# Optimization experiments

Measured on AMD Instinct MI355X. Metric: run time of the kernel, lower is better.

Reference implementation:

```python
import jax, jax.numpy as jnp
import numpy as np

B, T, D = 2, 2048, 1024
H = 4
KD = int(D * 0.5)      # total key dim = 512
VD = int(D * 1.0)      # total value dim = 1024
DK, DV = KD // H, VD // H  # per-head: 128, 256
CHUNK = 64
LOW_RANK = 16          # gate_low_rank_dim
NORMALIZER = 16.0      # gate_logit_normalizer
EPS = 1e-6


def setup_inputs() -> dict:
    key = jax.random.key(0)
    ks = jax.random.split(key, 10)
    def w(k, shape):
        return jax.random.normal(k, shape, jnp.float32) / np.sqrt(shape[0]).astype(np.float32)
    return {
        "x": jax.random.normal(ks[0], (B, T, D), jnp.float32),
        "Wq": w(ks[1], (D, KD)),
        "Wk": w(ks[2], (D, KD)),
        "Wv": w(ks[3], (D, VD)),
        "Wg": w(ks[4], (D, VD)),          # output gate projection
        "Wgk1": w(ks[5], (D, LOW_RANK)),  # low-rank gate proj (no bias)
        "Wgk2": w(ks[6], (LOW_RANK, KD)),
        "bgk2": jax.random.normal(ks[7], (KD,), jnp.float32) * 0.1,
        "gnorm_w": jnp.ones((DV,), jnp.float32),  # FusedRMSNormSwishGate weight
        "Wo": w(ks[8], (VD, D)),
    }


def reference(x, Wq, Wk, Wv, Wg, Wgk1, Wgk2, bgk2, gnorm_w, Wo):
    scale = DK ** -0.5
    NC = T // CHUNK
    # [B,T,d] -> [NC,B,H,C,d_head]
    to_heads = lambda a, d: a.reshape(B, NC, CHUNK, H, d).transpose(1, 0, 3, 2, 4)
    q = to_heads(x @ Wq, DK)
    k = to_heads(x @ Wk, DK)
    v = to_heads(x @ Wv, DV)
    # per-key log decay gate: logsigmoid(low-rank proj) / normalizer
    gk = jax.nn.log_sigmoid((x @ Wgk1) @ Wgk2 + bgk2) / NORMALIZER
    G = jnp.cumsum(to_heads(gk, DK), axis=3)  # inclusive cumsum within chunk

    def chunk_step(S, inp):
        k_c, v_c, G_c = inp                       # [B,H,C,DK],[B,H,C,DV],[B,H,C,DK]
        G_last = G_c[:, :, -1, :]                 # [B,H,DK] total chunk decay
        k_bar = k_c * jnp.exp(G_last[:, :, None, :] - G_c)  # decay pos->chunk end
        S_new = jnp.exp(G_last)[..., None] * S + jnp.einsum('bhck,bhcv->bhkv', k_bar, v_c)
        return S_new, S                           # emit state at chunk START

    S0 = jnp.zeros((B, H, DK, DV), x.dtype)
    _, S_prev = jax.lax.scan(chunk_step, S0, (k, v, G))  # [NC,B,H,DK,DV]

    qg = q * jnp.exp(G) * scale                   # decay-scaled queries
    o_inter = jnp.einsum('nbhck,nbhkv->nbhcv', qg, S_prev)
    kg = k * jnp.exp(-G)
    A = jnp.einsum('nbhik,nbhjk->nbhij', qg, kg)  # intra-chunk scores
    A = jnp.where(jnp.tril(jnp.ones((CHUNK, CHUNK), bool)), A, 0.0)
    o = o_inter + jnp.einsum('nbhij,nbhjv->nbhiv', A, v)  # [NC,B,H,C,DV]
    o = o.transpose(1, 0, 3, 2, 4).reshape(B, T, H, DV)

    # fused gated RMSNorm: rmsnorm(o)*weight * swish(g), then output proj
    g = (x @ Wg).reshape(B, T, H, DV)
    o = o * jax.lax.rsqrt(jnp.mean(o * o, axis=-1, keepdims=True) + EPS) * gnorm_w
    o = o * (g * jax.nn.sigmoid(g))
    return o.reshape(B, T, VD) @ Wo
```

## Files before the change

### kernel.cpp

```cpp
#include <hip/hip_runtime.h>
#include <hip/hip_bf16.h>

#define BDIM 2
#define TDIM 2048
#define DDIM 1024
#define HH 4
#define KD 512
#define VD 1024
#define DK 128
#define DV 256
#define NC 32
#define CHUNKC 64
#define MTOT (BDIM*TDIM)
#define NALL 3584
#define STRIDE_ST ((size_t)BDIM*HH*DK*DV)

typedef __bf16 bf16x8 __attribute__((ext_vector_type(8)));
typedef float  f32x4  __attribute__((ext_vector_type(4)));
typedef __hip_bfloat16 hbf;

__device__ __forceinline__ void async_copy16(const void* g, void* l) {
  __builtin_amdgcn_global_load_lds(
      (const __attribute__((address_space(1))) void*)g,
      (__attribute__((address_space(3))) void*)l, 16, 0, 0);
}

__global__ void cast_bf16_kernel(const float* __restrict__ src, hbf* __restrict__ dst) {
  int t = blockIdx.x*256 + threadIdx.x;
  float4 v = ((const float4*)src)[t];
  union { hbf h[4]; uint2 u; } o;
  o.h[0] = __float2bfloat16(v.x); o.h[1] = __float2bfloat16(v.y);
  o.h[2] = __float2bfloat16(v.z); o.h[3] = __float2bfloat16(v.w);
  ((uint2*)dst)[t] = o.u;
}

__global__ void prep_weights(const float* __restrict__ Wq, const float* __restrict__ Wk,
                             const float* __restrict__ Wv, const float* __restrict__ Wg,
                             const float* __restrict__ Wo, const float* __restrict__ W1,
                             const float* __restrict__ W2,
                             hbf* __restrict__ wtall, hbf* __restrict__ wto) {
  __shared__ float tile[32][33];
  const int n0 = blockIdx.x*32, k0 = blockIdx.y*32;
  const int tx = threadIdx.x & 31, ty = threadIdx.x >> 5;
  if (n0 >= 1024 && n0 < 1536) {
    #pragma unroll
    for (int r = ty; r < 32; r += 8) {
      int n = n0 - 1024 + r, k = k0 + tx;
      float s = 0.f;
      #pragma unroll
      for (int j = 0; j < 16; ++j) s += W1[(size_t)k*16 + j] * W2[(size_t)j*KD + n];
      wtall[(size_t)(n0 + r)*DDIM + k] = __float2bfloat16(s);
    }
    return;
  }
  const float* W; int Nsrc, nloc; hbf* outp; int orow;
  if      (n0 < 512)  { W = Wq; Nsrc = 512;  nloc = n0;        outp = wtall; orow = n0; }
  else if (n0 < 1024) { W = Wk; Nsrc = 512;  nloc = n0 - 512;  outp = wtall; orow = n0; }
  else if (n0 < 2560) { W = Wv; Nsrc = 1024; nloc = n0 - 1536; outp = wtall; orow = n0; }
  else if (n0 < 3584) { W = Wg; Nsrc = 1024; nloc = n0 - 2560; outp = wtall; orow = n0; }
  else                { W = Wo; Nsrc = 1024; nloc = n0 - 3584; outp = wto;   orow = n0 - 3584; }
  #pragma unroll
  for (int r = ty; r < 32; r += 8)
    tile[r][tx] = W[(size_t)(k0 + r)*Nsrc + nloc + tx];
  __syncthreads();
  #pragma unroll
  for (int r = ty; r < 32; r += 8)
    outp[(size_t)(orow + r)*DDIM + k0 + tx] = __float2bfloat16(tile[tx][r]);
}

template <int MODE>
__global__ __launch_bounds__(256) void gemm_bt(const hbf* __restrict__ A,
                                               const hbf* __restrict__ Bt,
                                               float* __restrict__ Cf,
                                               hbf* __restrict__ Cq,
                                               hbf* __restrict__ Cv,
                                               int M, int N, int K) {
  __shared__ hbf As0[128][32], As1[128][32];
  __shared__ hbf Bs0[128][32], Bs1[128][32];
  const int t = threadIdx.x;
  const int w = t >> 6, l = t & 63;
  const int lr = l >> 2;
  const int srcc = (((l & 3) - (l >> 4)) & 3) * 8;
  const int lane16 = l & 15, quad = l >> 4;
  const int sw = (lane16 >> 2) & 3;
  const int row0 = blockIdx.y*128, col0 = blockIdx.x*128;
  const int mb = (w >> 1)*64, nb = (w & 1)*64;

  const hbf* ga = A  + (size_t)(row0 + w*32 + lr)*K + srcc;
  const hbf* gb = Bt + (size_t)(col0 + w*32 + lr)*K + srcc;
  hbf* la0 = &As0[w*32][0];   hbf* la1 = &As0[w*32 + 16][0];
  hbf* la2 = &As1[w*32][0];   hbf* la3 = &As1[w*32 + 16][0];
  hbf* lb0 = &Bs0[w*32][0];   hbf* lb1 = &Bs0[w*32 + 16][0];
  hbf* lb2 = &Bs1[w*32][0];   hbf* lb3 = &Bs1[w*32 + 16][0];
  const size_t rstep = (size_t)16*K;

  f32x4 acc[4][4] = {};
  for (int k0 = 0; k0 < K; k0 += 64) {
    async_copy16(ga,              la0);
    async_copy16(ga + rstep,      la1);
    async_copy16(ga + 32,         la2);
    async_copy16(ga + rstep + 32, la3);
    async_copy16(gb,              lb0);
    async_copy16(gb + rstep,      lb1);
    async_copy16(gb + 32,         lb2);
    async_copy16(gb + rstep + 32, lb3);
    ga += 64; gb += 64;
    __syncthreads();
    {
      bf16x8 af[4], bfr[4];
      #pragma unroll
      for (int i = 0; i < 4; ++i)
        af[i] = *(const bf16x8*)&As0[mb + i*16 + lane16][((quad + sw) & 3)*8];
      #pragma unroll
      for (int j = 0; j < 4; ++j)
        bfr[j] = *(const bf16x8*)&Bs0[nb + j*16 + lane16][((quad + sw) & 3)*8];
      #pragma unroll
      for (int i = 0; i < 4; ++i)
        #pragma unroll
        for (int j = 0; j < 4; ++j)
          acc[i][j] = __builtin_amdgcn_mfma_f32_16x16x32_bf16(af[i], bfr[j], acc[i][j], 0, 0, 0);
    }
    {
      bf16x8 af[4], bfr[4];
      #pragma unroll
      for (int i = 0; i < 4; ++i)
        af[i] = *(const bf16x8*)&As1[mb + i*16 + lane16][((quad + sw) & 3)*8];
      #pragma unroll
      for (int j = 0; j < 4; ++j)
        bfr[j] = *(const bf16x8*)&Bs1[nb + j*16 + lane16][((quad + sw) & 3)*8];
      #pragma unroll
      for (int i = 0; i < 4; ++i)
        #pragma unroll
        for (int j = 0; j < 4; ++j)
          acc[i][j] = __builtin_amdgcn_mfma_f32_16x16x32_bf16(af[i], bfr[j], acc[i][j], 0, 0, 0);
    }
    __syncthreads();
  }
  #pragma unroll
  for (int i = 0; i < 4; ++i)
    #pragma unroll
    for (int j = 0; j < 4; ++j)
      #pragma unroll
      for (int r = 0; r < 4; ++r) {
        int m = row0 + mb + i*16 + quad*4 + r;
        int n = col0 + nb + j*16 + lane16;
        float v = acc[i][j][r];
        if (MODE == 0) {
          Cf[(size_t)m*N + n] = v;
        } else {
          if (n < 1024)       Cq[(size_t)m*1024 + n] = __float2bfloat16(v);
          else if (n < 1536)  Cf[(size_t)m*512  + n - 1024] = v;
          else                Cv[(size_t)m*2048 + n - 1536] = __float2bfloat16(v);
        }
      }
}

__global__ __launch_bounds__(256) void gate_kernel(const float* __restrict__ Gpre,
                                                   const hbf* __restrict__ qkbf,
                                                   const float* __restrict__ bias,
                                                   hbf* __restrict__ qgb,
                                                   hbf* __restrict__ kgb,
                                                   hbf* __restrict__ kbarb,
                                                   float* __restrict__ dec) {
  __shared__ float buf[CHUNKC][128];
  const int h  = blockIdx.x & 3;
  const int nc = (blockIdx.x >> 2) & 31;
  const int b  = blockIdx.x >> 7;
  const int t = threadIdx.x;
  const int bc = b*TDIM + nc*CHUNKC;
  const int col0 = h*128;
  #pragma unroll
  for (int i = 0; i < 32; ++i) {
    int idx = t + 256*i;
    int c = idx >> 7, col = idx & 127;
    float s = Gpre[(size_t)(bc + c)*KD + col0 + col] + bias[col0 + col];
    buf[c][col] = (fminf(s, 0.f) - log1pf(expf(-fabsf(s)))) * (1.0f/16.0f);
  }
  __syncthreads();
  if (t < 128) {
    float acc = 0.f;
    #pragma unroll
    for (int c = 0; c < CHUNKC; ++c) { acc += buf[c][t]; buf[c][t] = acc; }
    dec[((size_t)nc*8 + b*HH + h)*DK + t] = expf(acc);
  }
  __syncthreads();
  const float scale = 0.088388347648318447f;
  #pragma unroll
  for (int i = 0; i < 16; ++i) {
    int idx = t + 256*i;
    int c = idx >> 6, cp = (idx & 63)*2;
    float g0 = buf[c][cp], g1 = buf[c][cp + 1];
    float gl0 = buf[63][cp], gl1 = buf[63][cp + 1];
    const size_t qoff = (size_t)(bc + c)*1024 + col0 + cp;
    uint qu = *(const uint*)(qkbf + qoff);
    uint ku = *(const uint*)(qkbf + qoff + 512);
    float q0 = __bfloat162float(((const hbf*)&qu)[0]);
    float q1 = __bfloat162float(((const hbf*)&qu)[1]);
    float k0 = __bfloat162float(((const hbf*)&ku)[0]);
    float k1 = __bfloat162float(((const hbf*)&ku)[1]);
    union { hbf h2[2]; uint u; } o1, o2, o3;
    o1.h2[0] = __float2bfloat16(q0 * expf(g0) * scale);
    o1.h2[1] = __float2bfloat16(q1 * expf(g1) * scale);
    o2.h2[0] = __float2bfloat16(k0 * expf(-g0));
    o2.h2[1] = __float2bfloat16(k1 * expf(-g1));
    o3.h2[0] = __float2bfloat16(k0 * expf(gl0 - g0));
    o3.h2[1] = __float2bfloat16(k1 * expf(gl1 - g1));
    const size_t ooff = (size_t)(bc + c)*KD + col0 + cp;
    *(uint*)(qgb + ooff)   = o1.u;
    *(uint*)(kgb + ooff)   = o2.u;
    *(uint*)(kbarb + ooff) = o3.u;
  }
}

__global__ __launch_bounds__(256) void state_chunk_kernel(const hbf* __restrict__ kbarb,
                                                          const hbf* __restrict__ vgbf,
                                                          hbf* __restrict__ Ub) {
  const int bh = blockIdx.x & 7;
  const int nc = blockIdx.x >> 3;
  const int b = bh >> 2, h = bh & 3;
  const int t = threadIdx.x;
  const int w = t >> 6, l = t & 63;
  const int lane16 = l & 15, quad = l >> 4;
  __shared__ hbf kbarT[DK][72];
  __shared__ hbf vT[DV][72];
  const int bc = b*TDIM + nc*CHUNKC;
  #pragma unroll
  for (int i = 0; i < 32; ++i) {
    int idx = t + 256*i;
    int c = idx >> 7, kk = idx & 127;
    kbarT[kk][c] = kbarb[(size_t)(bc + c)*KD + h*DK + kk];
  }
  #pragma unroll
  for (int i = 0; i < 64; ++i) {
    int idx = t + 256*i;
    int c = idx >> 8, col = idx & 255;
    vT[col][c] = vgbf[(size_t)(bc + c)*2048 + h*DV + col];
  }
  __syncthreads();
  f32x4 acc[4][8] = {};
  #pragma unroll
  for (int kc = 0; kc < 2; ++kc) {
    bf16x8 av[4], bk[8];
    #pragma unroll
    for (int i = 0; i < 4; ++i)
      av[i] = *(const bf16x8*)&vT[w*64 + i*16 + lane16][kc*32 + quad*8];
    #pragma unroll
    for (int j = 0; j < 8; ++j)
      bk[j] = *(const bf16x8*)&kbarT[j*16 + lane16][kc*32 + quad*8];
    #pragma unroll
    for (int i = 0; i < 4; ++i)
      #pragma unroll
      for (int j = 0; j < 8; ++j)
        acc[i][j] = __builtin_amdgcn_mfma_f32_16x16x32_bf16(av[i], bk[j], acc[i][j], 0, 0, 0);
  }
  hbf* ub = Ub + ((size_t)nc*8 + bh)*((size_t)DK*DV);
  #pragma unroll
  for (int i = 0; i < 4; ++i)
    #pragma unroll
    for (int j = 0; j < 8; ++j)
      #pragma unroll
      for (int r = 0; r < 4; ++r) {
        int v = w*64 + i*16 + quad*4 + r;
        int k = j*16 + lane16;
        ub[(size_t)v*DK + k] = __float2bfloat16(acc[i][j][r]);
      }
}

__global__ __launch_bounds__(256) void state_scan_kernel(const hbf* __restrict__ Ub,
                                                         const float* __restrict__ dec,
                                                         hbf* __restrict__ Spb) {
  const int p = blockIdx.x*256 + threadIdx.x;
  const size_t e = (size_t)p*2;
  const int k = (int)(e & 127);
  const int bh = (int)(e >> 15);
  float S0 = 0.f, S1 = 0.f;
  for (int nc = 0; nc < NC; ++nc) {
    const size_t off = (size_t)nc*STRIDE_ST + e;
    uint uu = *(const uint*)(Ub + off);
    hbf u0 = *(const hbf*)&uu;
    hbf u1 = *((const hbf*)&uu + 1);
    union { hbf h[2]; uint u; } ov;
    ov.h[0] = __float2bfloat16(S0); ov.h[1] = __float2bfloat16(S1);
    *(uint*)(Spb + off) = ov.u;
    float2 d = *(const float2*)(dec + ((size_t)nc*8 + bh)*DK + k);
    S0 = S0 * d.x + __bfloat162float(u0);
    S1 = S1 * d.y + __bfloat162float(u1);
  }
}

__global__ __launch_bounds__(256) void out_kernel(const hbf* __restrict__ qgb,
                                                  const hbf* __restrict__ kgb,
                                                  const hbf* __restrict__ vgbf,
                                                  const hbf* __restrict__ Spb,
                                                  const float* __restrict__ gnw,
                                                  hbf* __restrict__ obf) {
  const int blk = blockIdx.x;
  const int h = blk & 3, b = (blk >> 2) & 1, nc = blk >> 3;
  const int t = threadIdx.x;
  const int w = t >> 6, l = t & 63;
  const int lane16 = l & 15, quad = l >> 4;

  __shared__ __align__(16) unsigned char smem[64768];
  hbf (*qgs)[136] = (hbf(*)[136])(smem);
  hbf (*Ald)[72]  = (hbf(*)[72]) (smem + 17408);
  hbf (*kgs)[136] = (hbf(*)[136])(smem + 26624);
  hbf (*vT)[72]   = (hbf(*)[72]) (smem + 26624);
  float* ssum     = (float*)     (smem + 63488);
  float* invb     = (float*)     (smem + 64512);

  const int bc = b*TDIM + nc*CHUNKC;

  #pragma unroll
  for (int i = 0; i < 4; ++i) {
    int idx = t + 256*i;
    int c = idx >> 4, ch = (idx & 15)*8;
    *(uint4*)&qgs[c][ch] = *(const uint4*)(qgb + (size_t)(bc + c)*KD + h*DK + ch);
    *(uint4*)&kgs[c][ch] = *(const uint4*)(kgb + (size_t)(bc + c)*KD + h*DK + ch);
  }
  __syncthreads();

  f32x4 acc1[4] = {};
  #pragma unroll
  for (int kc = 0; kc < 4; ++kc) {
    bf16x8 af = *(const bf16x8*)&qgs[w*16 + lane16][kc*32 + quad*8];
    #pragma unroll
    for (int j = 0; j < 4; ++j) {
      bf16x8 bf = *(const bf16x8*)&kgs[j*16 + lane16][kc*32 + quad*8];
      acc1[j] = __builtin_amdgcn_mfma_f32_16x16x32_bf16(af, bf, acc1[j], 0, 0, 0);
    }
  }
  __syncthreads();

  #pragma unroll
  for (int j = 0; j < 4; ++j)
    #pragma unroll
    for (int r = 0; r < 4; ++r) {
      int cr = w*16 + quad*4 + r;
      int cc = j*16 + lane16;
      Ald[cr][cc] = __float2bfloat16(cc <= cr ? acc1[j][r] : 0.f);
    }
  #pragma unroll
  for (int i = 0; i < 64; ++i) {
    int e = t + 256*i;
    int c = e >> 8, col = e & 255;
    vT[col][c] = vgbf[(size_t)(bc + c)*2048 + h*DV + col];
  }
  __syncthreads();

  const hbf* SpB = Spb + ((size_t)nc*8 + (b*HH + h))*((size_t)DK*DV);
  f32x4 acc[4][4] = {};
  #pragma unroll
  for (int kc = 0; kc < 4; ++kc) {
    bf16x8 af[4], bs[4];
    #pragma unroll
    for (int i = 0; i < 4; ++i)
      af[i] = *(const bf16x8*)&qgs[i*16 + lane16][kc*32 + quad*8];
    #pragma unroll
    for (int j = 0; j < 4; ++j) {
      int n = w*64 + j*16 + lane16;
      bs[j] = *(const bf16x8*)(SpB + (size_t)n*DK + kc*32 + quad*8);
    }
    #pragma unroll
    for (int i = 0; i < 4; ++i)
      #pragma unroll
      for (int j = 0; j < 4; ++j)
        acc[i][j] = __builtin_amdgcn_mfma_f32_16x16x32_bf16(af[i], bs[j], acc[i][j], 0, 0, 0);
  }
  #pragma unroll
  for (int kc = 0; kc < 2; ++kc) {
    bf16x8 aa[4], bv[4];
    #pragma unroll
    for (int i = 0; i < 4; ++i)
      aa[i] = *(const bf16x8*)&Ald[i*16 + lane16][kc*32 + quad*8];
    #pragma unroll
    for (int j = 0; j < 4; ++j)
      bv[j] = *(const bf16x8*)&vT[w*64 + j*16 + lane16][kc*32 + quad*8];
    #pragma unroll
    for (int i = 0; i < 4; ++i)
      #pragma unroll
      for (int j = 0; j < 4; ++j)
        acc[i][j] = __builtin_amdgcn_mfma_f32_16x16x32_bf16(aa[i], bv[j], acc[i][j], 0, 0, 0);
  }

  #pragma unroll
  for (int i = 0; i < 4; ++i)
    #pragma unroll
    for (int r = 0; r < 4; ++r) {
      float s = 0.f;
      #pragma unroll
      for (int j = 0; j < 4; ++j) s += acc[i][j][r]*acc[i][j][r];
      s += __shfl_xor(s, 1); s += __shfl_xor(s, 2);
      s += __shfl_xor(s, 4); s += __shfl_xor(s, 8);
      if (lane16 == 0) ssum[(i*16 + quad*4 + r)*4 + w] = s;
    }
  __syncthreads();
  if (t < 64) {
    float tot = ssum[t*4] + ssum[t*4+1] + ssum[t*4+2] + ssum[t*4+3];
    invb[t] = rsqrtf(tot * (1.0f/DV) + 1e-6f);
  }
  __syncthreads();
  float gnwv[4];
  #pragma unroll
  for (int j = 0; j < 4; ++j) gnwv[j] = gnw[w*64 + j*16 + lane16];
  #pragma unroll
  for (int i = 0; i < 4; ++i)
    #pragma unroll
    for (int r = 0; r < 4; ++r) {
      int m = i*16 + quad*4 + r;
      float inv = invb[m];
      size_t grow_ = (size_t)(bc + m)*2048 + 1024 + h*DV + w*64;
      size_t orow_ = (size_t)(bc + m)*VD + h*DV + w*64;
      #pragma unroll
      for (int j = 0; j < 4; ++j) {
        float gv = __bfloat162float(vgbf[grow_ + j*16 + lane16]);
        float sig = 1.f / (1.f + expf(-gv));
        float val = acc[i][j][r] * inv * gnwv[j];
        obf[orow_ + j*16 + lane16] = __float2bfloat16(val * (gv * sig));
      }
    }
}

extern "C" void kernel_launch(void* const* d_in, const int* in_sizes, int n_in,
                              void* d_out, int out_size, void* d_ws, size_t ws_size,
                              hipStream_t stream) {
  const float* x    = (const float*)d_in[0];
  const float* Wq   = (const float*)d_in[1];
  const float* Wk   = (const float*)d_in[2];
  const float* Wv   = (const float*)d_in[3];
  const float* Wg   = (const float*)d_in[4];
  const float* Wgk1 = (const float*)d_in[5];
  const float* Wgk2 = (const float*)d_in[6];
  const float* bgk2 = (const float*)d_in[7];
  const float* gnw  = (const float*)d_in[8];
  const float* Wo   = (const float*)d_in[9];
  float* out = (float*)d_out;

  float* ws  = (float*)d_ws;
  float* Gb  = ws;
  float* dec = Gb  + (size_t)MTOT*KD;
  hbf* xbf   = (hbf*)(dec + (size_t)NC*BDIM*HH*DK);
  hbf* wtall = xbf   + (size_t)MTOT*DDIM;
  hbf* wto   = wtall + (size_t)NALL*DDIM;
  hbf* qkbf  = wto   + (size_t)DDIM*DDIM;
  hbf* vgbf  = qkbf  + (size_t)MTOT*1024;
  hbf* qgb   = vgbf  + (size_t)MTOT*2048;
  hbf* kgb   = qgb   + (size_t)MTOT*KD;
  hbf* kbarb = kgb   + (size_t)MTOT*KD;
  hbf* Ub    = kbarb + (size_t)MTOT*KD;
  hbf* Spb   = Ub    + (size_t)NC*STRIDE_ST;
  hbf* obf   = Ub;

  cast_bf16_kernel<<<MTOT*DDIM/4/256, 256, 0, stream>>>(x, xbf);
  prep_weights<<<dim3(144, 32), 256, 0, stream>>>(Wq, Wk, Wv, Wg, Wo, Wgk1, Wgk2, wtall, wto);

  gemm_bt<1><<<dim3(NALL/128, MTOT/128), 256, 0, stream>>>(xbf, wtall, Gb, qkbf, vgbf, MTOT, NALL, DDIM);

  gate_kernel<<<256, 256, 0, stream>>>(Gb, qkbf, bgk2, qgb, kgb, kbarb, dec);
  state_chunk_kernel<<<NC*BDIM*HH, 256, 0, stream>>>(kbarb, vgbf, Ub);
  state_scan_kernel<<<(int)(STRIDE_ST/2/256), 256, 0, stream>>>(Ub, dec, Spb);
  out_kernel<<<NC*BDIM*HH, 256, 0, stream>>>(qgb, kgb, vgbf, Spb, gnw, obf);
  gemm_bt<0><<<dim3(DDIM/128, MTOT/128), 256, 0, stream>>>(obf, wto, out, (hbf*)nullptr, (hbf*)nullptr, MTOT, DDIM, DDIM);
}
```

Before: 231.0 us.

## Fuse prep kernels, merge gate with chunk-state kernel, add 64-row output GEMM

Result: faster. 219.5 us (-5.0%).

```diff
diff --git a/kernel.cpp b/kernel.cpp
--- a/kernel.cpp
+++ b/kernel.cpp
@@ -25,22 +25,24 @@
       (__attribute__((address_space(3))) void*)l, 16, 0, 0);
 }
 
-__global__ void cast_bf16_kernel(const float* __restrict__ src, hbf* __restrict__ dst) {
-  int t = blockIdx.x*256 + threadIdx.x;
-  float4 v = ((const float4*)src)[t];
-  union { hbf h[4]; uint2 u; } o;
-  o.h[0] = __float2bfloat16(v.x); o.h[1] = __float2bfloat16(v.y);
-  o.h[2] = __float2bfloat16(v.z); o.h[3] = __float2bfloat16(v.w);
-  ((uint2*)dst)[t] = o.u;
-}
-
-__global__ void prep_weights(const float* __restrict__ Wq, const float* __restrict__ Wk,
-                             const float* __restrict__ Wv, const float* __restrict__ Wg,
-                             const float* __restrict__ Wo, const float* __restrict__ W1,
-                             const float* __restrict__ W2,
-                             hbf* __restrict__ wtall, hbf* __restrict__ wto) {
+__global__ void fused_prep(const float* __restrict__ x, hbf* __restrict__ xbf,
+                           const float* __restrict__ Wq, const float* __restrict__ Wk,
+                           const float* __restrict__ Wv, const float* __restrict__ Wg,
+                           const float* __restrict__ Wo, const float* __restrict__ W1,
+                           const float* __restrict__ W2,
+                           hbf* __restrict__ wtall, hbf* __restrict__ wto) {
   __shared__ float tile[32][33];
-  const int n0 = blockIdx.x*32, k0 = blockIdx.y*32;
+  if (blockIdx.x < 4096) {
+    int t = blockIdx.x*256 + threadIdx.x;
+    float4 v = ((const float4*)x)[t];
+    union { hbf h[4]; uint2 u; } o;
+    o.h[0] = __float2bfloat16(v.x); o.h[1] = __float2bfloat16(v.y);
+    o.h[2] = __float2bfloat16(v.z); o.h[3] = __float2bfloat16(v.w);
+    ((uint2*)xbf)[t] = o.u;
+    return;
+  }
+  const int bb = blockIdx.x - 4096;
+  const int n0 = (bb % 144)*32, k0 = (bb / 144)*32;
   const int tx = threadIdx.x & 31, ty = threadIdx.x >> 5;
   if (n0 >= 1024 && n0 < 1536) {
     #pragma unroll
@@ -155,81 +157,130 @@
       }
 }
 
-__global__ __launch_bounds__(256) void gate_kernel(const float* __restrict__ Gpre,
-                                                   const hbf* __restrict__ qkbf,
-                                                   const float* __restrict__ bias,
-                                                   hbf* __restrict__ qgb,
-                                                   hbf* __restrict__ kgb,
-                                                   hbf* __restrict__ kbarb,
-                                                   float* __restrict__ dec) {
-  __shared__ float buf[CHUNKC][128];
-  const int h  = blockIdx.x & 3;
-  const int nc = (blockIdx.x >> 2) & 31;
-  const int b  = blockIdx.x >> 7;
+__global__ __launch_bounds__(256) void gemm_out(const hbf* __restrict__ A,
+                                                const hbf* __restrict__ Bt,
+                                                float* __restrict__ Cf,
+                                                int M, int N, int K) {
+  __shared__ hbf As0[64][32], As1[64][32];
+  __shared__ hbf Bs0[128][32], Bs1[128][32];
   const int t = threadIdx.x;
-  const int bc = b*TDIM + nc*CHUNKC;
-  const int col0 = h*128;
-  #pragma unroll
-  for (int i = 0; i < 32; ++i) {
-    int idx = t + 256*i;
-    int c = idx >> 7, col = idx & 127;
-    float s = Gpre[(size_t)(bc + c)*KD + col0 + col] + bias[col0 + col];
-    buf[c][col] = (fminf(s, 0.f) - log1pf(expf(-fabsf(s)))) * (1.0f/16.0f);
-  }
-  __syncthreads();
-  if (t < 128) {
-    float acc = 0.f;
-    #pragma unroll
-    for (int c = 0; c < CHUNKC; ++c) { acc += buf[c][t]; buf[c][t] = acc; }
-    dec[((size_t)nc*8 + b*HH + h)*DK + t] = expf(acc);
-  }
-  __syncthreads();
-  const float scale = 0.088388347648318447f;
-  #pragma unroll
-  for (int i = 0; i < 16; ++i) {
-    int idx = t + 256*i;
-    int c = idx >> 6, cp = (idx & 63)*2;
-    float g0 = buf[c][cp], g1 = buf[c][cp + 1];
-    float gl0 = buf[63][cp], gl1 = buf[63][cp + 1];
-    const size_t qoff = (size_t)(bc + c)*1024 + col0 + cp;
-    uint qu = *(const uint*)(qkbf + qoff);
-    uint ku = *(const uint*)(qkbf + qoff + 512);
-    float q0 = __bfloat162float(((const hbf*)&qu)[0]);
-    float q1 = __bfloat162float(((const hbf*)&qu)[1]);
-    float k0 = __bfloat162float(((const hbf*)&ku)[0]);
-    float k1 = __bfloat162float(((const hbf*)&ku)[1]);
-    union { hbf h2[2]; uint u; } o1, o2, o3;
-    o1.h2[0] = __float2bfloat16(q0 * expf(g0) * scale);
-    o1.h2[1] = __float2bfloat16(q1 * expf(g1) * scale);
-    o2.h2[0] = __float2bfloat16(k0 * expf(-g0));
-    o2.h2[1] = __float2bfloat16(k1 * expf(-g1));
-    o3.h2[0] = __float2bfloat16(k0 * expf(gl0 - g0));
-    o3.h2[1] = __float2bfloat16(k1 * expf(gl1 - g1));
-    const size_t ooff = (size_t)(bc + c)*KD + col0 + cp;
-    *(uint*)(qgb + ooff)   = o1.u;
-    *(uint*)(kgb + ooff)   = o2.u;
-    *(uint*)(kbarb + ooff) = o3.u;
-  }
-}
-
-__global__ __launch_bounds__(256) void state_chunk_kernel(const hbf* __restrict__ kbarb,
-                                                          const hbf* __restrict__ vgbf,
-                                                          hbf* __restrict__ Ub) {
+  const int w = t >> 6, l = t & 63;
+  const int lr = l >> 2;
+  const int srcc = (((l & 3) - (l >> 4)) & 3) * 8;
+  const int lane16 = l & 15, quad = l >> 4;
+  const int sw = (lane16 >> 2) & 3;
+  const int row0 = blockIdx.y*64, col0 = blockIdx.x*128;
+  const int mb = (w >> 1)*32, nb = (w & 1)*64;
+
+  const hbf* ga = A  + (size_t)(row0 + w*16 + lr)*K + srcc;
+  const hbf* gb = Bt + (size_t)(col0 + w*32 + lr)*K + srcc;
+  hbf* la0 = &As0[w*16][0];   hbf* la1 = &As1[w*16][0];
+  hbf* lb0 = &Bs0[w*32][0];   hbf* lb1 = &Bs0[w*32 + 16][0];
+  hbf* lb2 = &Bs1[w*32][0];   hbf* lb3 = &Bs1[w*32 + 16][0];
+  const size_t rstep = (size_t)16*K;
+
+  f32x4 acc[2][4] = {};
+  for (int k0 = 0; k0 < K; k0 += 64) {
+    async_copy16(ga,              la0);
+    async_copy16(ga + 32,         la1);
+    async_copy16(gb,              lb0);
+    async_copy16(gb + rstep,      lb1);
+    async_copy16(gb + 32,         lb2);
+    async_copy16(gb + rstep + 32, lb3);
+    ga += 64; gb += 64;
+    __syncthreads();
+    {
+      bf16x8 af[2], bfr[4];
+      #pragma unroll
+      for (int i = 0; i < 2; ++i)
+        af[i] = *(const bf16x8*)&As0[mb + i*16 + lane16][((quad + sw) & 3)*8];
+      #pragma unroll
+      for (int j = 0; j < 4; ++j)
+        bfr[j] = *(const bf16x8*)&Bs0[nb + j*16 + lane16][((quad + sw) & 3)*8];
+      #pragma unroll
+      for (int i = 0; i < 2; ++i)
+        #pragma unroll
+        for (int j = 0; j < 4; ++j)
+          acc[i][j] = __builtin_amdgcn_mfma_f32_16x16x32_bf16(af[i], bfr[j], acc[i][j], 0, 0, 0);
+    }
+    {
+      bf16x8 af[2], bfr[4];
+      #pragma unroll
+      for (int i = 0; i < 2; ++i)
+        af[i] = *(const bf16x8*)&As1[mb + i*16 + lane16][((quad + sw) & 3)*8];
+      #pragma unroll
+      for (int j = 0; j < 4; ++j)
+        bfr[j] = *(const bf16x8*)&Bs1[nb + j*16 + lane16][((quad + sw) & 3)*8];
+      #pragma unroll
+      for (int i = 0; i < 2; ++i)
+        #pragma unroll
+        for (int j = 0; j < 4; ++j)
+          acc[i][j] = __builtin_amdgcn_mfma_f32_16x16x32_bf16(af[i], bfr[j], acc[i][j], 0, 0, 0);
+    }
+    __syncthreads();
+  }
+  #pragma unroll
+  for (int i = 0; i < 2; ++i)
+    #pragma unroll
+    for (int j = 0; j < 4; ++j)
+      #pragma unroll
+      for (int r = 0; r < 4; ++r) {
+        int m = row0 + mb + i*16 + quad*4 + r;
+        int n = col0 + nb + j*16 + lane16;
+        Cf[(size_t)m*N + n] = acc[i][j][r];
+      }
+}
+
+__global__ __launch_bounds__(256) void gate_chunk_kernel(const float* __restrict__ Gpre,
+                                                         const hbf* __restrict__ qkbf,
+                                                         const hbf* __restrict__ vgbf,
+                                                         const float* __restrict__ bias,
+                                                         hbf* __restrict__ qgb,
+                                                         hbf* __restrict__ kgb,
+                                                         hbf* __restrict__ Ub,
+                                                         float* __restrict__ dec) {
   const int bh = blockIdx.x & 7;
   const int nc = blockIdx.x >> 3;
   const int b = bh >> 2, h = bh & 3;
   const int t = threadIdx.x;
   const int w = t >> 6, l = t & 63;
   const int lane16 = l & 15, quad = l >> 4;
-  __shared__ hbf kbarT[DK][72];
-  __shared__ hbf vT[DV][72];
+  __shared__ __align__(16) unsigned char smem[55808];
+  float (*buf)[128] = (float(*)[128])(smem);
+  hbf (*vT)[72]     = (hbf(*)[72])  (smem);
+  hbf (*kbarT)[72]  = (hbf(*)[72])  (smem + 36864);
   const int bc = b*TDIM + nc*CHUNKC;
+  const int col0 = h*DK;
   #pragma unroll
   for (int i = 0; i < 32; ++i) {
     int idx = t + 256*i;
     int c = idx >> 7, kk = idx & 127;
-    kbarT[kk][c] = kbarb[(size_t)(bc + c)*KD + h*DK + kk];
-  }
+    float s = Gpre[(size_t)(bc + c)*KD + col0 + kk] + bias[col0 + kk];
+    buf[c][kk] = (fminf(s, 0.f) - log1pf(expf(-fabsf(s)))) * (1.0f/16.0f);
+  }
+  __syncthreads();
+  if (t < 128) {
+    float acc = 0.f;
+    #pragma unroll
+    for (int c = 0; c < CHUNKC; ++c) { acc += buf[c][t]; buf[c][t] = acc; }
+    dec[((size_t)nc*8 + bh)*DK + t] = expf(acc);
+  }
+  __syncthreads();
+  const float scale = 0.088388347648318447f;
+  #pragma unroll
+  for (int i = 0; i < 32; ++i) {
+    int idx = t + 256*i;
+    int c = idx >> 7, kk = idx & 127;
+    float g = buf[c][kk], gl = buf[63][kk];
+    const size_t qoff = (size_t)(bc + c)*1024 + col0 + kk;
+    float qv = __bfloat162float(qkbf[qoff]);
+    float kv = __bfloat162float(qkbf[qoff + 512]);
+    const size_t ooff = (size_t)(bc + c)*KD + col0 + kk;
+    qgb[ooff] = __float2bfloat16(qv * expf(g) * scale);
+    kgb[ooff] = __float2bfloat16(kv * expf(-g));
+    kbarT[kk][c] = __float2bfloat16(kv * expf(gl - g));
+  }
+  __syncthreads();
   #pragma unroll
   for (int i = 0; i < 64; ++i) {
     int idx = t + 256*i;
@@ -445,19 +496,16 @@
   hbf* vgbf  = qkbf  + (size_t)MTOT*1024;
   hbf* qgb   = vgbf  + (size_t)MTOT*2048;
   hbf* kgb   = qgb   + (size_t)MTOT*KD;
-  hbf* kbarb = kgb   + (size_t)MTOT*KD;
-  hbf* Ub    = kbarb + (size_t)MTOT*KD;
+  hbf* Ub    = kgb   + (size_t)MTOT*KD;
   hbf* Spb   = Ub    + (size_t)NC*STRIDE_ST;
   hbf* obf   = Ub;
 
-  cast_bf16_kernel<<<MTOT*DDIM/4/256, 256, 0, stream>>>(x, xbf);
-  prep_weights<<<dim3(144, 32), 256, 0, stream>>>(Wq, Wk, Wv, Wg, Wo, Wgk1, Wgk2, wtall, wto);
+  fused_prep<<<4096 + 4608, 256, 0, stream>>>(x, xbf, Wq, Wk, Wv, Wg, Wo, Wgk1, Wgk2, wtall, wto);
 
   gemm_bt<1><<<dim3(NALL/128, MTOT/128), 256, 0, stream>>>(xbf, wtall, Gb, qkbf, vgbf, MTOT, NALL, DDIM);
 
-  gate_kernel<<<256, 256, 0, stream>>>(Gb, qkbf, bgk2, qgb, kgb, kbarb, dec);
-  state_chunk_kernel<<<NC*BDIM*HH, 256, 0, stream>>>(kbarb, vgbf, Ub);
+  gate_chunk_kernel<<<NC*BDIM*HH, 256, 0, stream>>>(Gb, qkbf, vgbf, bgk2, qgb, kgb, Ub, dec);
   state_scan_kernel<<<(int)(STRIDE_ST/2/256), 256, 0, stream>>>(Ub, dec, Spb);
   out_kernel<<<NC*BDIM*HH, 256, 0, stream>>>(qgb, kgb, vgbf, Spb, gnw, obf);
-  gemm_bt<0><<<dim3(DDIM/128, MTOT/128), 256, 0, stream>>>(obf, wto, out, (hbf*)nullptr, (hbf*)nullptr, MTOT, DDIM, DDIM);
-}
+  gemm_out<<<dim3(DDIM/128, MTOT/64), 256, 0, stream>>>(obf, wto, out, MTOT, DDIM, DDIM);
+}
```
